# Kernel tuning notes

Hardware: AMD Instinct MI355X
Metric: run time of the kernel (lower is better)

The kernel has to match this reference:

```python
import jax, jax.numpy as jnp
import numpy as np
from math import sqrt

B, C, L = 32, 32, 512            # batch, channels(enc_in), seq_len
INTRA, INTER = 1024, 256          # memory-bank intra_len, inter_len
DCP, DDE = 64, 512                # compress width (retrieved set size), denoise hidden
SCALE = 0.05


def setup_inputs() -> dict:
    key = jax.random.key(0)
    ks = jax.random.split(key, 12)
    s = 0.02  # small init scale for weights
    return {
        "x_loc": jax.random.normal(ks[0], (B, C, L), jnp.float32),
        "indices": jax.random.randint(ks[1], (B, L), 0, INTRA),
        "map_raw": jax.random.normal(ks[2], (C, INTRA, INTER), jnp.float32),
        # compress: Linear(INTER->DCP), ReLU, Linear(DCP->DCP)
        "cW1": jax.random.normal(ks[3], (DCP, INTER), jnp.float32) * s,
        "cb1": jnp.zeros((DCP,), jnp.float32),
        "cW2": jax.random.normal(ks[4], (DCP, DCP), jnp.float32) * s,
        "cb2": jnp.zeros((DCP,), jnp.float32),
        # denoise: Linear(INTRA->DDE), ReLU, Linear(DDE->INTRA)
        "dW1": jax.random.normal(ks[5], (DDE, INTRA), jnp.float32) * s,
        "db1": jnp.zeros((DDE,), jnp.float32),
        "dW2": jax.random.normal(ks[6], (INTRA, DDE), jnp.float32) * s,
        "db2": jnp.zeros((INTRA,), jnp.float32),
        "lamda1": jnp.zeros((C, 1), jnp.float32),
        "lamda2": jnp.zeros((1, L), jnp.float32),
    }


def reference(x_loc, indices, map_raw, cW1, cb1, cW2, cb2,
              dW1, db1, dW2, db2, lamda1, lamda2):
    # compress along inter_len: (C, INTRA, INTER) -> (C, INTRA, DCP)
    map_tmp = jax.nn.relu(map_raw @ cW1.T + cb1) @ cW2.T + cb2
    map_tmp = jnp.swapaxes(map_tmp, 1, 2)            # (C, DCP, INTRA)
    # denoise along intra_len
    map_st = jax.nn.relu(map_tmp @ dW1.T + db1) @ dW2.T + db2  # (C, DCP, INTRA)
    # gather: map_dy[b,c,d,l] = map_st[c, d, indices[b,l]]
    map_dy = jnp.transpose(map_st[:, :, indices], (2, 0, 1, 3))  # (B, C, DCP, L)
    # l1 similarity (negative L1 distance, scaled by sqrt(L))
    scores = -jnp.sum(jnp.abs(x_loc[:, :, None, :] - map_dy), axis=-1) / sqrt(L)  # (B,C,DCP)
    scores = jax.nn.softmax(scores * SCALE, axis=2)
    lamda = jax.nn.sigmoid(lamda1) @ jax.nn.sigmoid(lamda2)     # (C, L)
    x_global = jnp.einsum('bchl,bch->bcl', map_dy, scores)      # (B, C, L)
    return x_global * lamda + x_loc * (1.0 - lamda)
```

## Files before the change

kernel.cpp:

```cpp
#include <hip/hip_runtime.h>
#include <hip/hip_bf16.h>

#define Bn 32
#define Cn 32
#define Ln 512
#define INTRA 1024
#define INTER 256
#define DCP 64
#define DDE 512
#define SCALEF 0.05f

typedef __attribute__((ext_vector_type(8))) short short8;
typedef __attribute__((ext_vector_type(4))) float floatx4;

__device__ __forceinline__ short bf16_of(float f) {
    union { float f; unsigned u; } v; v.f = f;
    unsigned r = (v.u + 0x7FFFu + ((v.u >> 16) & 1u)) >> 16;
    return (short)r;
}

__global__ __launch_bounds__(256) void prep_weights(
    const float* __restrict__ cW1, const float* __restrict__ cW2,
    const float* __restrict__ dW1, const float* __restrict__ dW2,
    short* __restrict__ cW1b, short* __restrict__ cW2b,
    short* __restrict__ dW1b, short* __restrict__ dW2b)
{
    int i = blockIdx.x * 256 + threadIdx.x;
    if (i < 64 * 256) cW1b[i] = bf16_of(cW1[i]);
    if (i < 64 * 64)  cW2b[i] = bf16_of(cW2[i]);
    if (i < DDE * INTRA) { dW1b[i] = bf16_of(dW1[i]); dW2b[i] = bf16_of(dW2[i]); }
}

__global__ __launch_bounds__(256) void compress_fused(
    const float* __restrict__ map_raw, const short* __restrict__ cW1b,
    const float* __restrict__ cb1, const short* __restrict__ cW2b,
    const float* __restrict__ cb2, short* __restrict__ M1T)
{
    const int c  = blockIdx.y;
    const int m0 = blockIdx.x * 64;
    const float* A = map_raw + (long)c * INTRA * INTER + (long)m0 * INTER;

    __shared__ short lds[64 * 32 + 64 * 32 + 64 * 64];
    short* Asb = lds;
    short* Bsb = lds + 2048;
    short* Tsb = lds + 4096;

    const int t    = threadIdx.x;
    const int w    = t >> 6;
    const int lane = t & 63;
    const int ln   = lane & 15;
    const int quad = lane >> 4;
    const int sr = t >> 2;
    const int sk = (t & 3) * 8;

    floatx4 acc[4] = {};

    float4 a0 = *(const float4*)(A + sr * INTER + sk);
    float4 a1 = *(const float4*)(A + sr * INTER + sk + 4);
    short8 bpre = *(const short8*)(cW1b + sr * INTER + sk);

    for (int k0 = 0; k0 < INTER; k0 += 32) {
        __syncthreads();
        short8 av;
        av[0] = bf16_of(a0.x); av[1] = bf16_of(a0.y);
        av[2] = bf16_of(a0.z); av[3] = bf16_of(a0.w);
        av[4] = bf16_of(a1.x); av[5] = bf16_of(a1.y);
        av[6] = bf16_of(a1.z); av[7] = bf16_of(a1.w);
        *(short8*)&Asb[sr * 32 + sk] = av;
        *(short8*)&Bsb[sr * 32 + sk] = bpre;
        __syncthreads();

        if (k0 + 32 < INTER) {
            a0 = *(const float4*)(A + sr * INTER + k0 + 32 + sk);
            a1 = *(const float4*)(A + sr * INTER + k0 + 32 + sk + 4);
            bpre = *(const short8*)(cW1b + sr * INTER + k0 + 32 + sk);
        }

        short8 af = *(const short8*)&Asb[(w * 16 + ln) * 32 + quad * 8];
        #pragma unroll
        for (int nt = 0; nt < 4; ++nt) {
            short8 bf = *(const short8*)&Bsb[(nt * 16 + ln) * 32 + quad * 8];
            acc[nt] = __builtin_amdgcn_mfma_f32_16x16x32_bf16(af, bf, acc[nt], 0, 0, 0);
        }
    }

    __syncthreads();

    #pragma unroll
    for (int nt = 0; nt < 4; ++nt) {
        const int n = nt * 16 + ln;
        const float b = cb1[n];
        #pragma unroll
        for (int r = 0; r < 4; ++r) {
            const int m = w * 16 + quad * 4 + r;
            Tsb[m * 64 + n] = bf16_of(fmaxf(acc[nt][r] + b, 0.f));
        }
    }
    {
        const int n = t >> 2, kc = (t & 3) * 16;
        *(short8*)&lds[n * 64 + kc]     = *(const short8*)(cW2b + n * 64 + kc);
        *(short8*)&lds[n * 64 + kc + 8] = *(const short8*)(cW2b + n * 64 + kc + 8);
    }
    __syncthreads();

    floatx4 acc2[4] = {};
    #pragma unroll
    for (int ks = 0; ks < 2; ++ks) {
        short8 af = *(const short8*)&Tsb[(w * 16 + ln) * 64 + ks * 32 + quad * 8];
        #pragma unroll
        for (int nt = 0; nt < 4; ++nt) {
            short8 bf = *(const short8*)&lds[(nt * 16 + ln) * 64 + ks * 32 + quad * 8];
            acc2[nt] = __builtin_amdgcn_mfma_f32_16x16x32_bf16(af, bf, acc2[nt], 0, 0, 0);
        }
    }

    short* out = M1T + (long)c * 64 * INTRA;
    #pragma unroll
    for (int nt = 0; nt < 4; ++nt) {
        const int n = nt * 16 + ln;
        const float b = cb2[n];
        short t0 = bf16_of(acc2[nt][0] + b);
        short t1 = bf16_of(acc2[nt][1] + b);
        short t2 = bf16_of(acc2[nt][2] + b);
        short t3 = bf16_of(acc2[nt][3] + b);
        const int m = m0 + w * 16 + quad * 4;
        *(short4*)(out + (long)n * INTRA + m) = make_short4(t0, t1, t2, t3);
    }
}

template <int RELU, int OUT_TBF16>
__global__ __launch_bounds__(256) void gemm_mfma(
    const short* __restrict__ A, const short* __restrict__ Bt,
    const float* __restrict__ biasM, void* __restrict__ Cout,
    int M, int K)
{
    const int c  = blockIdx.y;
    const int m0 = blockIdx.x * 64;
    const short* Bc = Bt + (long)c * 64 * K;

    __shared__ short Asb[64 * 32];
    __shared__ short Bsb[64 * 32];

    const int t    = threadIdx.x;
    const int w    = t >> 6;
    const int lane = t & 63;
    const int ln   = lane & 15;
    const int quad = lane >> 4;
    const int sr = t >> 2;
    const int sk = (t & 3) * 8;

    floatx4 acc[4] = {};
    short8 apre = *(const short8*)(A + (long)(m0 + sr) * K + sk);
    short8 bpre = *(const short8*)(Bc + (long)sr * K + sk);

    for (int k0 = 0; k0 < K; k0 += 32) {
        __syncthreads();
        *(short8*)&Asb[sr * 32 + sk] = apre;
        *(short8*)&Bsb[sr * 32 + sk] = bpre;
        __syncthreads();
        const int kn = k0 + 32;
        if (kn < K) {
            apre = *(const short8*)(A + (long)(m0 + sr) * K + kn + sk);
            bpre = *(const short8*)(Bc + (long)sr * K + kn + sk);
        }
        short8 af = *(const short8*)&Asb[(w * 16 + ln) * 32 + quad * 8];
        #pragma unroll
        for (int nt = 0; nt < 4; ++nt) {
            short8 bf = *(const short8*)&Bsb[(nt * 16 + ln) * 32 + quad * 8];
            acc[nt] = __builtin_amdgcn_mfma_f32_16x16x32_bf16(af, bf, acc[nt], 0, 0, 0);
        }
    }

    float bm[4];
    #pragma unroll
    for (int r = 0; r < 4; ++r) bm[r] = biasM[m0 + w * 16 + quad * 4 + r];

    if (OUT_TBF16) {
        short* out = (short*)Cout + (long)c * 64 * M;
        #pragma unroll
        for (int nt = 0; nt < 4; ++nt) {
            const int n = nt * 16 + ln;
            short t0, t1, t2, t3;
            float v0 = acc[nt][0] + bm[0], v1 = acc[nt][1] + bm[1];
            float v2 = acc[nt][2] + bm[2], v3 = acc[nt][3] + bm[3];
            if (RELU) { v0 = fmaxf(v0, 0.f); v1 = fmaxf(v1, 0.f);
                        v2 = fmaxf(v2, 0.f); v3 = fmaxf(v3, 0.f); }
            t0 = bf16_of(v0); t1 = bf16_of(v1); t2 = bf16_of(v2); t3 = bf16_of(v3);
            const int m = m0 + w * 16 + quad * 4;
            *(short4*)(out + (long)n * M + m) = make_short4(t0, t1, t2, t3);
        }
    } else {
        float* out = (float*)Cout + (long)c * (long)M * 64;
        #pragma unroll
        for (int nt = 0; nt < 4; ++nt) {
            const int n = nt * 16 + ln;
            #pragma unroll
            for (int r = 0; r < 4; ++r) {
                float v = acc[nt][r] + bm[r];
                if (RELU) v = fmaxf(v, 0.f);
                out[(long)(m0 + w * 16 + quad * 4 + r) * 64 + n] = v;
            }
        }
    }
}

__global__ __launch_bounds__(256) void fuse_kernel(
    const float* __restrict__ x_loc, const int* __restrict__ indices,
    const float* __restrict__ S, const float* __restrict__ lamda1,
    const float* __restrict__ lamda2, float* __restrict__ out)
{
    const int c = blockIdx.x;
    const int b = blockIdx.y;

    __shared__ float xs[Ln];
    __shared__ int   idx[Ln];
    __shared__ float red[4][DCP];
    __shared__ float w[DCP];

    const int t = threadIdx.x;
    const float* xp = x_loc + ((long)b * Cn + c) * Ln;
    const int*   ip = indices + (long)b * Ln;
    xs[t]        = xp[t];
    xs[t + 256]  = xp[t + 256];
    idx[t]       = ip[t];
    idx[t + 256] = ip[t + 256];
    __syncthreads();

    const float* Sc = S + (long)c * INTRA * DCP;

    const int lane = t & 63;
    const int grp  = t >> 6;
    float s = 0.f;
    for (int l = grp; l < Ln; l += 4) {
        float g = Sc[idx[l] * DCP + lane];
        s += fabsf(xs[l] - g);
    }
    red[grp][lane] = s;
    __syncthreads();

    if (t < DCP) {
        float sc = red[0][t] + red[1][t] + red[2][t] + red[3][t];
        sc = -sc * (SCALEF * 0.044194173824159216f);
        float m = sc;
        #pragma unroll
        for (int o = 32; o > 0; o >>= 1) m = fmaxf(m, __shfl_xor(m, o));
        float e = __expf(sc - m);
        float ssum = e;
        #pragma unroll
        for (int o = 32; o > 0; o >>= 1) ssum += __shfl_xor(ssum, o);
        w[t] = e / ssum;
    }
    __syncthreads();

    const float lam1 = 1.f / (1.f + __expf(-lamda1[c]));
    for (int l = t; l < Ln; l += 256) {
        const float* row = Sc + (long)idx[l] * DCP;
        float acc = 0.f;
        #pragma unroll
        for (int d = 0; d < DCP; d += 4) {
            float4 g = *(const float4*)&row[d];
            acc = fmaf(g.x, w[d],     acc);
            acc = fmaf(g.y, w[d + 1], acc);
            acc = fmaf(g.z, w[d + 2], acc);
            acc = fmaf(g.w, w[d + 3], acc);
        }
        float lam = lam1 * (1.f / (1.f + __expf(-lamda2[l])));
        out[((long)b * Cn + c) * Ln + l] = acc * lam + xs[l] * (1.f - lam);
    }
}

extern "C" void kernel_launch(void* const* d_in, const int* in_sizes, int n_in,
                              void* d_out, int out_size, void* d_ws, size_t ws_size,
                              hipStream_t stream)
{
    const float* x_loc   = (const float*)d_in[0];
    const int*   indices = (const int*)d_in[1];
    const float* map_raw = (const float*)d_in[2];
    const float* cW1     = (const float*)d_in[3];
    const float* cb1     = (const float*)d_in[4];
    const float* cW2     = (const float*)d_in[5];
    const float* cb2     = (const float*)d_in[6];
    const float* dW1     = (const float*)d_in[7];
    const float* db1     = (const float*)d_in[8];
    const float* dW2     = (const float*)d_in[9];
    const float* db2     = (const float*)d_in[10];
    const float* lamda1  = (const float*)d_in[11];
    const float* lamda2  = (const float*)d_in[12];
    float* out = (float*)d_out;

    short* wsS  = (short*)d_ws;
    short* cW1b = wsS;
    short* cW2b = cW1b + 16384;
    short* dW1b = cW2b + 4096;
    short* dW2b = dW1b + 524288;
    short* M1T  = dW2b + 524288;
    short* HT   = M1T + 2097152;
    float* S    = (float*)(HT + 1048576);

    prep_weights<<<2048, 256, 0, stream>>>(cW1, cW2, dW1, dW2,
                                           cW1b, cW2b, dW1b, dW2b);

    compress_fused<<<dim3(INTRA / 64, Cn), 256, 0, stream>>>(
        map_raw, cW1b, cb1, cW2b, cb2, M1T);

    gemm_mfma<1, 1><<<dim3(DDE / 64, Cn), 256, 0, stream>>>(
        dW1b, M1T, db1, (void*)HT, DDE, INTRA);

    gemm_mfma<0, 0><<<dim3(INTRA / 64, Cn), 256, 0, stream>>>(
        dW2b, HT, db2, (void*)S, INTRA, DDE);

    fuse_kernel<<<dim3(Cn, Bn), 256, 0, stream>>>(
        x_loc, indices, S, lamda1, lamda2, out);
}
```

Before: 169.7 us.

## Store denoised map as bf16, widen GEMM K-tiles, reshape fuse gather

The generic GEMM template becomes two specialized kernels. Each stages 64-wide K tiles in padded LDS, which halves the number of barriers and is meant to avoid bank conflicts. The final denoise output S is now written in bf16 instead of fp32, which halves the gather traffic in fuse_kernel. The weighted-sum phase changes from a per-thread row dot product to lane-per-channel gathers with wave shuffle reductions. This adds shuffle overhead and some bf16 rounding error in the retrieved map values.

```diff
diff --git a/kernel.cpp b/kernel.cpp
--- a/kernel.cpp
+++ b/kernel.cpp
@@ -18,6 +18,11 @@
     unsigned r = (v.u + 0x7FFFu + ((v.u >> 16) & 1u)) >> 16;
     return (short)r;
 }
+__device__ __forceinline__ float f_of_bf16(short h) {
+    union { unsigned u; float f; } v;
+    v.u = ((unsigned)(unsigned short)h) << 16;
+    return v.f;
+}
 
 __global__ __launch_bounds__(256) void prep_weights(
     const float* __restrict__ cW1, const float* __restrict__ cW2,
@@ -114,7 +119,7 @@
         }
     }
 
-    short* out = M1T + (long)c * 64 * INTRA;
+    short* outp = M1T + (long)c * 64 * INTRA;
     #pragma unroll
     for (int nt = 0; nt < 4; ++nt) {
         const int n = nt * 16 + ln;
@@ -124,89 +129,137 @@
         short t2 = bf16_of(acc2[nt][2] + b);
         short t3 = bf16_of(acc2[nt][3] + b);
         const int m = m0 + w * 16 + quad * 4;
-        *(short4*)(out + (long)n * INTRA + m) = make_short4(t0, t1, t2, t3);
-    }
-}
-
-template <int RELU, int OUT_TBF16>
-__global__ __launch_bounds__(256) void gemm_mfma(
-    const short* __restrict__ A, const short* __restrict__ Bt,
-    const float* __restrict__ biasM, void* __restrict__ Cout,
-    int M, int K)
+        *(short4*)(outp + (long)n * INTRA + m) = make_short4(t0, t1, t2, t3);
+    }
+}
+
+__global__ __launch_bounds__(256) void gemm_dn1(
+    const short* __restrict__ A, const short* __restrict__ M1T,
+    const float* __restrict__ db1, short* __restrict__ HT)
 {
     const int c  = blockIdx.y;
     const int m0 = blockIdx.x * 64;
-    const short* Bc = Bt + (long)c * 64 * K;
-
-    __shared__ short Asb[64 * 32];
-    __shared__ short Bsb[64 * 32];
-
-    const int t    = threadIdx.x;
-    const int w    = t >> 6;
-    const int lane = t & 63;
-    const int ln   = lane & 15;
-    const int quad = lane >> 4;
-    const int sr = t >> 2;
-    const int sk = (t & 3) * 8;
+    const short* Bc = M1T + (long)c * 64 * INTRA;
+
+    __shared__ short Asb[64 * 72];
+    __shared__ short Bsb[64 * 72];
+
+    const int t = threadIdx.x, w = t >> 6, lane = t & 63;
+    const int ln = lane & 15, quad = lane >> 4;
+    const int sr = t >> 2, sk = (t & 3) * 16;
 
     floatx4 acc[4] = {};
-    short8 apre = *(const short8*)(A + (long)(m0 + sr) * K + sk);
-    short8 bpre = *(const short8*)(Bc + (long)sr * K + sk);
-
-    for (int k0 = 0; k0 < K; k0 += 32) {
-        __syncthreads();
-        *(short8*)&Asb[sr * 32 + sk] = apre;
-        *(short8*)&Bsb[sr * 32 + sk] = bpre;
-        __syncthreads();
-        const int kn = k0 + 32;
-        if (kn < K) {
-            apre = *(const short8*)(A + (long)(m0 + sr) * K + kn + sk);
-            bpre = *(const short8*)(Bc + (long)sr * K + kn + sk);
-        }
-        short8 af = *(const short8*)&Asb[(w * 16 + ln) * 32 + quad * 8];
+    short8 a0 = *(const short8*)(A + (long)(m0 + sr) * INTRA + sk);
+    short8 a1 = *(const short8*)(A + (long)(m0 + sr) * INTRA + sk + 8);
+    short8 b0 = *(const short8*)(Bc + (long)sr * INTRA + sk);
+    short8 b1 = *(const short8*)(Bc + (long)sr * INTRA + sk + 8);
+
+    for (int k0 = 0; k0 < INTRA; k0 += 64) {
+        __syncthreads();
+        *(short8*)&Asb[sr * 72 + sk]     = a0;
+        *(short8*)&Asb[sr * 72 + sk + 8] = a1;
+        *(short8*)&Bsb[sr * 72 + sk]     = b0;
+        *(short8*)&Bsb[sr * 72 + sk + 8] = b1;
+        __syncthreads();
+        const int kn = k0 + 64;
+        if (kn < INTRA) {
+            a0 = *(const short8*)(A + (long)(m0 + sr) * INTRA + kn + sk);
+            a1 = *(const short8*)(A + (long)(m0 + sr) * INTRA + kn + sk + 8);
+            b0 = *(const short8*)(Bc + (long)sr * INTRA + kn + sk);
+            b1 = *(const short8*)(Bc + (long)sr * INTRA + kn + sk + 8);
+        }
+        short8 af0 = *(const short8*)&Asb[(w * 16 + ln) * 72 + quad * 8];
+        short8 af1 = *(const short8*)&Asb[(w * 16 + ln) * 72 + 32 + quad * 8];
         #pragma unroll
         for (int nt = 0; nt < 4; ++nt) {
-            short8 bf = *(const short8*)&Bsb[(nt * 16 + ln) * 32 + quad * 8];
-            acc[nt] = __builtin_amdgcn_mfma_f32_16x16x32_bf16(af, bf, acc[nt], 0, 0, 0);
+            short8 bf0 = *(const short8*)&Bsb[(nt * 16 + ln) * 72 + quad * 8];
+            short8 bf1 = *(const short8*)&Bsb[(nt * 16 + ln) * 72 + 32 + quad * 8];
+            acc[nt] = __builtin_amdgcn_mfma_f32_16x16x32_bf16(af0, bf0, acc[nt], 0, 0, 0);
+            acc[nt] = __builtin_amdgcn_mfma_f32_16x16x32_bf16(af1, bf1, acc[nt], 0, 0, 0);
         }
     }
 
     float bm[4];
     #pragma unroll
-    for (int r = 0; r < 4; ++r) bm[r] = biasM[m0 + w * 16 + quad * 4 + r];
-
-    if (OUT_TBF16) {
-        short* out = (short*)Cout + (long)c * 64 * M;
+    for (int r = 0; r < 4; ++r) bm[r] = db1[m0 + w * 16 + quad * 4 + r];
+
+    short* outp = HT + (long)c * 64 * DDE;
+    #pragma unroll
+    for (int nt = 0; nt < 4; ++nt) {
+        const int n = nt * 16 + ln;
+        float v0 = fmaxf(acc[nt][0] + bm[0], 0.f);
+        float v1 = fmaxf(acc[nt][1] + bm[1], 0.f);
+        float v2 = fmaxf(acc[nt][2] + bm[2], 0.f);
+        float v3 = fmaxf(acc[nt][3] + bm[3], 0.f);
+        const int m = m0 + w * 16 + quad * 4;
+        *(short4*)(outp + (long)n * DDE + m) =
+            make_short4(bf16_of(v0), bf16_of(v1), bf16_of(v2), bf16_of(v3));
+    }
+}
+
+__global__ __launch_bounds__(256) void gemm_dn2(
+    const short* __restrict__ HT, const short* __restrict__ dW2b,
+    const float* __restrict__ db2, short* __restrict__ S16)
+{
+    const int c  = blockIdx.y;
+    const int n0 = blockIdx.x * 64;
+    const short* A = HT + (long)c * 64 * DDE;
+    const short* B = dW2b + (long)n0 * DDE;
+
+    __shared__ short Asb[64 * 72];
+    __shared__ short Bsb[64 * 72];
+
+    const int t = threadIdx.x, w = t >> 6, lane = t & 63;
+    const int ln = lane & 15, quad = lane >> 4;
+    const int sr = t >> 2, sk = (t & 3) * 16;
+
+    floatx4 acc[4] = {};
+    short8 a0 = *(const short8*)(A + (long)sr * DDE + sk);
+    short8 a1 = *(const short8*)(A + (long)sr * DDE + sk + 8);
+    short8 b0 = *(const short8*)(B + (long)sr * DDE + sk);
+    short8 b1 = *(const short8*)(B + (long)sr * DDE + sk + 8);
+
+    for (int k0 = 0; k0 < DDE; k0 += 64) {
+        __syncthreads();
+        *(short8*)&Asb[sr * 72 + sk]     = a0;
+        *(short8*)&Asb[sr * 72 + sk + 8] = a1;
+        *(short8*)&Bsb[sr * 72 + sk]     = b0;
+        *(short8*)&Bsb[sr * 72 + sk + 8] = b1;
+        __syncthreads();
+        const int kn = k0 + 64;
+        if (kn < DDE) {
+            a0 = *(const short8*)(A + (long)sr * DDE + kn + sk);
+            a1 = *(const short8*)(A + (long)sr * DDE + kn + sk + 8);
+            b0 = *(const short8*)(B + (long)sr * DDE + kn + sk);
+            b1 = *(const short8*)(B + (long)sr * DDE + kn + sk + 8);
+        }
+        short8 af0 = *(const short8*)&Asb[(w * 16 + ln) * 72 + quad * 8];
+        short8 af1 = *(const short8*)&Asb[(w * 16 + ln) * 72 + 32 + quad * 8];
         #pragma unroll
         for (int nt = 0; nt < 4; ++nt) {
-            const int n = nt * 16 + ln;
-            short t0, t1, t2, t3;
-            float v0 = acc[nt][0] + bm[0], v1 = acc[nt][1] + bm[1];
-            float v2 = acc[nt][2] + bm[2], v3 = acc[nt][3] + bm[3];
-            if (RELU) { v0 = fmaxf(v0, 0.f); v1 = fmaxf(v1, 0.f);
-                        v2 = fmaxf(v2, 0.f); v3 = fmaxf(v3, 0.f); }
-            t0 = bf16_of(v0); t1 = bf16_of(v1); t2 = bf16_of(v2); t3 = bf16_of(v3);
-            const int m = m0 + w * 16 + quad * 4;
-            *(short4*)(out + (long)n * M + m) = make_short4(t0, t1, t2, t3);
-        }
-    } else {
-        float* out = (float*)Cout + (long)c * (long)M * 64;
-        #pragma unroll
-        for (int nt = 0; nt < 4; ++nt) {
-            const int n = nt * 16 + ln;
-            #pragma unroll
-            for (int r = 0; r < 4; ++r) {
-                float v = acc[nt][r] + bm[r];
-                if (RELU) v = fmaxf(v, 0.f);
-                out[(long)(m0 + w * 16 + quad * 4 + r) * 64 + n] = v;
-            }
-        }
+            short8 bf0 = *(const short8*)&Bsb[(nt * 16 + ln) * 72 + quad * 8];
+            short8 bf1 = *(const short8*)&Bsb[(nt * 16 + ln) * 72 + 32 + quad * 8];
+            acc[nt] = __builtin_amdgcn_mfma_f32_16x16x32_bf16(af0, bf0, acc[nt], 0, 0, 0);
+            acc[nt] = __builtin_amdgcn_mfma_f32_16x16x32_bf16(af1, bf1, acc[nt], 0, 0, 0);
+        }
+    }
+
+    #pragma unroll
+    for (int nt = 0; nt < 4; ++nt) {
+        const int n = n0 + nt * 16 + ln;
+        const float bb = db2[n];
+        const int m = w * 16 + quad * 4;
+        short t0 = bf16_of(acc[nt][0] + bb);
+        short t1 = bf16_of(acc[nt][1] + bb);
+        short t2 = bf16_of(acc[nt][2] + bb);
+        short t3 = bf16_of(acc[nt][3] + bb);
+        *(short4*)(S16 + ((long)c * INTRA + n) * DCP + m) = make_short4(t0, t1, t2, t3);
     }
 }
 
 __global__ __launch_bounds__(256) void fuse_kernel(
     const float* __restrict__ x_loc, const int* __restrict__ indices,
-    const float* __restrict__ S, const float* __restrict__ lamda1,
+    const short* __restrict__ S16, const float* __restrict__ lamda1,
     const float* __restrict__ lamda2, float* __restrict__ out)
 {
     const int c = blockIdx.x;
@@ -215,7 +268,7 @@
     __shared__ float xs[Ln];
     __shared__ int   idx[Ln];
     __shared__ float red[4][DCP];
-    __shared__ float w[DCP];
+    __shared__ float wsm[DCP];
 
     const int t = threadIdx.x;
     const float* xp = x_loc + ((long)b * Cn + c) * Ln;
@@ -226,13 +279,14 @@
     idx[t + 256] = ip[t + 256];
     __syncthreads();
 
-    const float* Sc = S + (long)c * INTRA * DCP;
+    const short* Sc = S16 + (long)c * INTRA * DCP;
 
     const int lane = t & 63;
     const int grp  = t >> 6;
+
     float s = 0.f;
     for (int l = grp; l < Ln; l += 4) {
-        float g = Sc[idx[l] * DCP + lane];
+        float g = f_of_bf16(Sc[idx[l] * DCP + lane]);
         s += fabsf(xs[l] - g);
     }
     red[grp][lane] = s;
@@ -248,24 +302,29 @@
         float ssum = e;
         #pragma unroll
         for (int o = 32; o > 0; o >>= 1) ssum += __shfl_xor(ssum, o);
-        w[t] = e / ssum;
-    }
-    __syncthreads();
-
+        wsm[t] = e / ssum;
+    }
+    __syncthreads();
+
+    const float wgt  = wsm[lane];
     const float lam1 = 1.f / (1.f + __expf(-lamda1[c]));
-    for (int l = t; l < Ln; l += 256) {
-        const float* row = Sc + (long)idx[l] * DCP;
-        float acc = 0.f;
-        #pragma unroll
-        for (int d = 0; d < DCP; d += 4) {
-            float4 g = *(const float4*)&row[d];
-            acc = fmaf(g.x, w[d],     acc);
-            acc = fmaf(g.y, w[d + 1], acc);
-            acc = fmaf(g.z, w[d + 2], acc);
-            acc = fmaf(g.w, w[d + 3], acc);
-        }
-        float lam = lam1 * (1.f / (1.f + __expf(-lamda2[l])));
-        out[((long)b * Cn + c) * Ln + l] = acc * lam + xs[l] * (1.f - lam);
+
+    #pragma unroll
+    for (int j = 0; j < 2; ++j) {
+        const int lbase = grp * 128 + j * 64;
+        float res = 0.f;
+        #pragma unroll 8
+        for (int i = 0; i < 64; ++i) {
+            const int l = lbase + i;
+            float g = f_of_bf16(Sc[idx[l] * DCP + lane]);
+            float v = wgt * g;
+            #pragma unroll
+            for (int o = 32; o > 0; o >>= 1) v += __shfl_xor(v, o);
+            if (lane == i) res = v;
+        }
+        const int l = lbase + lane;
+        const float lam = lam1 * (1.f / (1.f + __expf(-lamda2[l])));
+        out[((long)b * Cn + c) * Ln + l] = res * lam + xs[l] * (1.f - lam);
     }
 }
 
@@ -295,7 +354,7 @@
     short* dW2b = dW1b + 524288;
     short* M1T  = dW2b + 524288;
     short* HT   = M1T + 2097152;
-    float* S    = (float*)(HT + 1048576);
+    short* S16  = HT + 1048576;
 
     prep_weights<<<2048, 256, 0, stream>>>(cW1, cW2, dW1, dW2,
                                            cW1b, cW2b, dW1b, dW2b);
@@ -303,12 +362,12 @@
     compress_fused<<<dim3(INTRA / 64, Cn), 256, 0, stream>>>(
         map_raw, cW1b, cb1, cW2b, cb2, M1T);
 
-    gemm_mfma<1, 1><<<dim3(DDE / 64, Cn), 256, 0, stream>>>(
-        dW1b, M1T, db1, (void*)HT, DDE, INTRA);
-
-    gemm_mfma<0, 0><<<dim3(INTRA / 64, Cn), 256, 0, stream>>>(
-        dW2b, HT, db2, (void*)S, INTRA, DDE);
+    gemm_dn1<<<dim3(DDE / 64, Cn), 256, 0, stream>>>(
+        dW1b, M1T, db1, HT);
+
+    gemm_dn2<<<dim3(INTRA / 64, Cn), 256, 0, stream>>>(
+        HT, dW2b, db2, S16);
 
     fuse_kernel<<<dim3(Cn, Bn), 256, 0, stream>>>(
-        x_loc, indices, S, lamda1, lamda2, out);
-}
+        x_loc, indices, S16, lamda1, lamda2, out);
+}
```

Result: slower. 190.8 us (+12.4%).
